# Kernel tuning notes

Hardware: AMD Instinct MI355X
Metric: run time of the kernel (lower is better)

## Reference

```python
import jax, jax.numpy as jnp
import numpy as np

N, K, B, D, T = 30000, 32, 8, 256, 10
NC = T + 1            # int_small_classes
LB_COL, UB_COL = 21, 22
INF = 1e18


def _ln(x, g, b, eps=1e-5):
    m = jnp.mean(x, axis=-1, keepdims=True)
    v = jnp.mean((x - m) ** 2, axis=-1, keepdims=True)
    return (x - m) * jax.lax.rsqrt(v + eps) * g + b


def _head(x, ng, nb, W1, b1, W2, b2, Wh, bh):
    # LayerNorm -> Linear -> GELU -> Linear -> GELU -> residual -> head (dropout off: eval)
    h = _ln(x, ng, nb)
    h = jax.nn.gelu(h @ W1.T + b1, approximate=False)
    h = jax.nn.gelu(h @ W2.T + b2, approximate=False)
    return (x + h) @ Wh.T + bh


def setup_inputs():
    key = jax.random.key(0)
    ks = jax.random.split(key, 32)
    s = 0.05
    inp = {}
    inp['evolved_tokens'] = jax.random.normal(ks[0], (B * K, D), jnp.float32)
    inp['var_batch'] = jnp.sort(jax.random.randint(ks[1], (N,), 0, B))
    aw = jax.random.uniform(ks[2], (N, K), jnp.float32)
    inp['attn_weights'] = aw / aw.sum(-1, keepdims=True)
    inp['var_types'] = jax.random.randint(ks[3], (N,), 0, 3)
    inp['z_var_0'] = jax.random.normal(ks[4], (N, D), jnp.float32)
    vf = 0.1 * jax.random.normal(ks[5], (N, 23), jnp.float32)
    lb = jnp.floor(jax.random.uniform(ks[6], (N,), minval=-5.0, maxval=0.0))
    ub = lb + jnp.floor(jax.random.uniform(ks[7], (N,), minval=0.0, maxval=30.0))
    ub = jnp.where(jax.random.uniform(ks[8], (N,)) < 0.1, 1e19, ub)
    inp['variable_features'] = vf.at[:, LB_COL].set(lb).at[:, UB_COL].set(ub)
    # deslice proj + fusion norm
    inp['Wp'] = s * jax.random.normal(ks[9], (D, D), jnp.float32)
    inp['bp'] = jnp.zeros((D,), jnp.float32)
    inp['fn_g'] = jnp.ones((D,), jnp.float32)
    inp['fn_b'] = jnp.zeros((D,), jnp.float32)
    # three decoder heads
    i = 10
    for name, out in (('bin', 1), ('ints', NC), ('intl', 1)):
        inp[name + '_ng'] = jnp.ones((D,), jnp.float32)
        inp[name + '_nb'] = jnp.zeros((D,), jnp.float32)
        inp[name + '_W1'] = s * jax.random.normal(ks[i], (D, D), jnp.float32)
        inp[name + '_b1'] = jnp.zeros((D,), jnp.float32)
        inp[name + '_W2'] = s * jax.random.normal(ks[i + 1], (D, D), jnp.float32)
        inp[name + '_b2'] = jnp.zeros((D,), jnp.float32)
        inp[name + '_Wh'] = s * jax.random.normal(ks[i + 2], (out, D), jnp.float32)
        inp[name + '_bh'] = (jnp.full((out,), -0.5, jnp.float32) if name == 'bin'
                             else jnp.zeros((out,), jnp.float32))
        i += 3
    return inp


def reference(evolved_tokens, var_batch, attn_weights, var_types, z_var_0,
              variable_features, Wp, bp, fn_g, fn_b,
              bin_ng, bin_nb, bin_W1, bin_b1, bin_W2, bin_b2, bin_Wh, bin_bh,
              ints_ng, ints_nb, ints_W1, ints_b1, ints_W2, ints_b2, ints_Wh, ints_bh,
              intl_ng, intl_nb, intl_W1, intl_b1, intl_W2, intl_b2, intl_Wh, intl_bh):
    # 1. deslice: attn_weights @ projected evolved tokens of the variable's graph
    proj = evolved_tokens @ Wp.T + bp          # [B*K, D]
    tok3 = proj.reshape(B, K, D)
    z_des = jnp.einsum('nk,nkd->nd', attn_weights, tok3[var_batch])  # [N, D]
    # 2. residual fusion + LayerNorm
    z_out = _ln(z_des + z_var_0, fn_g, fn_b)
    # 3. routing (extract_int_routing)
    lb = variable_features[:, LB_COL]
    ub = variable_features[:, UB_COL]
    is_int = var_types == 2
    finite = (jnp.abs(lb) < INF) & (jnp.abs(ub) < INF)
    mask_int_small = is_int & finite & ((ub - lb) <= T)
    mask_int_large = is_int & ~mask_int_small
    mask_bin = var_types == 1
    offsets = jnp.floor(lb)                                   # [N]
    ranges = jnp.clip(jnp.ceil(ub) - offsets + 1.0, 1.0, NC).astype(jnp.int32)  # [N]
    # 4. decode. Heads are evaluated densely on all N rows; the original's
    #    gather->MLP->scatter equals row-selection of these dense outputs.
    prob_bin = jax.nn.sigmoid(_head(z_out, bin_ng, bin_nb, bin_W1, bin_b1,
                                    bin_W2, bin_b2, bin_Wh, bin_bh))   # [N, 1]
    logits = _head(z_out, ints_ng, ints_nb, ints_W1, ints_b1,
                   ints_W2, ints_b2, ints_Wh, ints_bh)                 # [N, NC]
    valid = jnp.arange(NC)[None, :] < ranges[:, None]
    logits = jnp.where(valid, logits, -1e9)  # dynamic logit masking of invalid classes
    pred_large = _head(z_out, intl_ng, intl_nb, intl_W1, intl_b1,
                       intl_W2, intl_b2, intl_Wh, intl_bh)             # [N, 1]
    return (z_out, prob_bin, logits, pred_large,
            mask_bin, mask_int_small, mask_int_large, offsets, ranges)
```

## Files before the change

kernel.cpp:

```cpp
#include <hip/hip_runtime.h>
#include <math.h>

#define NV   30000
#define DD   256
#define KK   32
#define NCLS 11
#define NT   469
#define NT2  938

#define OZ  0
#define OPB 7680000
#define OLG 7710000
#define OPL 8040000
#define OMB 8070000
#define OMS 8100000
#define OML 8130000
#define OOF 8160000
#define ORG 8190000

typedef __bf16 bf16x8 __attribute__((ext_vector_type(8)));
typedef float  f32x4  __attribute__((ext_vector_type(4)));

__device__ __forceinline__ unsigned short f2b(float f) {
    unsigned u = __float_as_uint(f);
    u += 0x7fffu + ((u >> 16) & 1u);
    return (unsigned short)(u >> 16);
}

__device__ __forceinline__ float gelu_f(float x) {
    float x2 = x * x;
    float m = x * __builtin_fmaf(-0.0713548163f, x2, -1.5957691216f);
    float e = __expf(m);
    return x * __builtin_amdgcn_rcpf(1.0f + e);
}

__device__ __forceinline__ int swz(int row) {
    int r = row & 31;
    return (r + (r >> 3)) & 7;
}
__device__ __forceinline__ int lidx(int row, int col) {
    return row * 256 + ((((col) >> 3) ^ swz(row)) << 3) + (col & 7);
}
__device__ __forceinline__ int physchunk(int ck, int row) {
    return (ck & ~7) | ((ck & 7) ^ swz(row));
}

struct WP {
    const float *W1, *ng, *nb, *b1, *W2, *Wh;
    unsigned short *W1e, *W2b, *Whb;
    float *b1e, *swh;
    int nc;
};

__global__ void k_prep(const float* __restrict__ et, const float* __restrict__ Wp,
                       const float* __restrict__ bp, unsigned short* __restrict__ projT,
                       const float* __restrict__ vf, const int* __restrict__ vt,
                       float* __restrict__ out,
                       WP wa, WP wb, WP wc) {
    __shared__ float es[DD];
    __shared__ float red[4], red2[4];
    if (blockIdx.y == 0) {
        int r = blockIdx.x, c = threadIdx.x;
        es[c] = et[r * DD + c];
        __syncthreads();
        const float4* w4 = (const float4*)(Wp + c * DD);
        float acc = bp[c];
#pragma unroll 16
        for (int d = 0; d < DD / 4; ++d) {
            float4 w = w4[d];
            acc += es[4 * d] * w.x + es[4 * d + 1] * w.y + es[4 * d + 2] * w.z + es[4 * d + 3] * w.w;
        }
        projT[c * DD + r] = f2b(acc);
        return;
    }
    if (blockIdx.y == 4) {
        int n = blockIdx.x * 256 + threadIdx.x;
        if (n < NV) {
            float lb = vf[n * 23 + 21], ub = vf[n * 23 + 22];
            int t = vt[n];
            bool is_int = (t == 2);
            bool finite = (fabsf(lb) < 1e18f) && (fabsf(ub) < 1e18f);
            bool small_ = is_int && finite && (ub - lb <= 10.0f);
            float off = floorf(lb);
            float rngf = ceilf(ub) - off + 1.0f;
            rngf = fminf(fmaxf(rngf, 1.0f), (float)NCLS);
            out[OMB + n] = (t == 1) ? 1.0f : 0.0f;
            out[OMS + n] = small_ ? 1.0f : 0.0f;
            out[OML + n] = (is_int && !small_) ? 1.0f : 0.0f;
            out[OOF + n] = off;
            out[ORG + n] = (float)((int)rngf);
        }
        return;
    }
    WP wp = (blockIdx.y == 1) ? wa : ((blockIdx.y == 2) ? wb : wc);
    int j = blockIdx.x, d = threadIdx.x;
    float v1 = wp.W1[j * DD + d];
    wp.W1e[j * DD + d] = f2b(v1 * wp.ng[d]);
    wp.W2b[j * DD + d] = f2b(wp.W2[j * DD + d]);
    float p2 = 0.f;
    if (j < 16) {
        p2 = (j < wp.nc) ? wp.Wh[j * DD + d] : 0.f;
        wp.Whb[j * DD + d] = f2b(p2);
    }
    float p = v1 * wp.nb[d];
#pragma unroll
    for (int m = 1; m < 64; m <<= 1) { p += __shfl_xor(p, m); p2 += __shfl_xor(p2, m); }
    if ((d & 63) == 0) { red[d >> 6] = p; red2[d >> 6] = p2; }
    __syncthreads();
    if (d == 0) {
        wp.b1e[j] = wp.b1[j] + red[0] + red[1] + red[2] + red[3];
        if (j < 16) wp.swh[j] = red2[0] + red2[1] + red2[2] + red2[3];
    }
}

__global__ __launch_bounds__(512)
void k_zout(const unsigned short* __restrict__ projT, const int* __restrict__ vb,
            const float* __restrict__ aw, const float* __restrict__ z0,
            const float* __restrict__ g, const float* __restrict__ b,
            const unsigned short* __restrict__ Whb, const float* __restrict__ swh,
            float* __restrict__ out, unsigned short* __restrict__ zhat,
            float* __restrict__ zwhT) {
    __shared__ unsigned short Al[64 * 256];
    __shared__ float sqs[64 * 8], sqq[64 * 8];
    __shared__ float mvm[64], mvr[64], sig[64];
    __shared__ float gs[DD], bs[DD];
    __shared__ float swhs[48];
    int tid = threadIdx.x;
    int lane = tid & 63, wv = tid >> 6;
    int l15 = lane & 15, lq = lane >> 4;
    int n0 = blockIdx.x * 64;

    if (tid < 256) gs[tid] = g[tid];
    else           bs[tid - 256] = b[tid - 256];
    if (tid < 48) swhs[tid] = swh[tid];
    {
        uint4 z4 = make_uint4(0, 0, 0, 0);
        uint4* dst = (uint4*)Al;
#pragma unroll
        for (int j = 0; j < 4; ++j) dst[tid + j * 512] = z4;
    }
    __syncthreads();
    {
        int r = tid >> 3, sub = tid & 7;
        int n = n0 + r;
        if (n < NV) {
            int bb = vb[n];
            float4 a4 = *(const float4*)(aw + (size_t)n * KK + sub * 4);
            int j0 = bb * 32 + sub * 4;
            int phys = r * 256 + (physchunk(j0 >> 3, r) << 3) + (j0 & 7);
            ushort4 u;
            u.x = f2b(a4.x); u.y = f2b(a4.y); u.z = f2b(a4.z); u.w = f2b(a4.w);
            *(ushort4*)(Al + phys) = u;
        }
    }
    __syncthreads();

    int nb0 = wv * 32;
    f32x4 acc[4][2];
#pragma unroll
    for (int mt = 0; mt < 4; ++mt)
#pragma unroll
        for (int nt = 0; nt < 2; ++nt) acc[mt][nt] = f32x4{0.f, 0.f, 0.f, 0.f};

    {
        const unsigned short* Bb = projT + (size_t)(nb0 + l15) * DD + lq * 8;
        bf16x8 bfr[2][2], afr[4];
#pragma unroll
        for (int nt = 0; nt < 2; ++nt) bfr[0][nt] = *(const bf16x8*)(Bb + nt * 16 * DD);
#pragma unroll
        for (int ks = 0; ks < 8; ++ks) {
            int cur = ks & 1;
            if (ks < 7) {
#pragma unroll
                for (int nt = 0; nt < 2; ++nt)
                    bfr[cur ^ 1][nt] = *(const bf16x8*)(Bb + nt * 16 * DD + (ks + 1) * 32);
            }
            int ck = ks * 4 + lq;
#pragma unroll
            for (int mt = 0; mt < 4; ++mt) {
                int row = mt * 16 + l15;
                afr[mt] = *(const bf16x8*)(Al + row * 256 + (physchunk(ck, row) << 3));
            }
#pragma unroll
            for (int nt = 0; nt < 2; ++nt)
#pragma unroll
                for (int mt = 0; mt < 4; ++mt)
                    acc[mt][nt] = __builtin_amdgcn_mfma_f32_16x16x32_bf16(afr[mt], bfr[cur][nt], acc[mt][nt], 0, 0, 0);
        }
    }
#pragma unroll
    for (int mt = 0; mt < 4; ++mt)
#pragma unroll
        for (int nt = 0; nt < 2; ++nt) {
            int col = nb0 + nt * 16 + l15;
#pragma unroll
            for (int r = 0; r < 4; ++r) {
                int n = n0 + mt * 16 + lq * 4 + r;
                float zv = (n < NV) ? z0[(size_t)n * DD + col] : 0.f;
                acc[mt][nt][r] += zv;
            }
        }
#pragma unroll
    for (int mt = 0; mt < 4; ++mt)
#pragma unroll
        for (int r = 0; r < 4; ++r) {
            float s = acc[mt][0][r] + acc[mt][1][r];
            float q = acc[mt][0][r] * acc[mt][0][r] + acc[mt][1][r] * acc[mt][1][r];
#pragma unroll
            for (int m = 1; m < 16; m <<= 1) { s += __shfl_xor(s, m); q += __shfl_xor(q, m); }
            if (l15 == 0) { int row = mt * 16 + lq * 4 + r; sqs[row * 8 + wv] = s; sqq[row * 8 + wv] = q; }
        }
    __syncthreads();
    if (tid < 64) {
        float s = 0.f, q = 0.f;
#pragma unroll
        for (int w = 0; w < 8; ++w) { s += sqs[tid * 8 + w]; q += sqq[tid * 8 + w]; }
        float mean = s * (1.f / DD);
        float var  = q * (1.f / DD) - mean * mean;
        mvm[tid] = mean; mvr[tid] = rsqrtf(var + 1e-5f);
    }
    __syncthreads();
    float zb[4][2][4];
#pragma unroll
    for (int mt = 0; mt < 4; ++mt)
#pragma unroll
        for (int nt = 0; nt < 2; ++nt) {
            int col = nb0 + nt * 16 + l15;
#pragma unroll
            for (int r = 0; r < 4; ++r) {
                int row = mt * 16 + lq * 4 + r;
                float z = (acc[mt][nt][r] - mvm[row]) * mvr[row] * gs[col] + bs[col];
                zb[mt][nt][r] = z;
                int n = n0 + row;
                if (n < NV) out[OZ + (size_t)n * DD + col] = z;
            }
        }
#pragma unroll
    for (int mt = 0; mt < 4; ++mt)
#pragma unroll
        for (int r = 0; r < 4; ++r) {
            float s = zb[mt][0][r] + zb[mt][1][r];
            float q = zb[mt][0][r] * zb[mt][0][r] + zb[mt][1][r] * zb[mt][1][r];
#pragma unroll
            for (int m = 1; m < 16; m <<= 1) { s += __shfl_xor(s, m); q += __shfl_xor(q, m); }
            if (l15 == 0) { int row = mt * 16 + lq * 4 + r; sqs[row * 8 + wv] = s; sqq[row * 8 + wv] = q; }
        }
    __syncthreads();
    if (tid < 64) {
        float s = 0.f, q = 0.f;
#pragma unroll
        for (int w = 0; w < 8; ++w) { s += sqs[tid * 8 + w]; q += sqq[tid * 8 + w]; }
        float m2 = s * (1.f / DD);
        float v2 = q * (1.f / DD) - m2 * m2;
        float r2 = rsqrtf(v2 + 1e-5f);
        mvm[tid] = m2; mvr[tid] = r2; sig[tid] = (v2 + 1e-5f) * r2;
    }
    __syncthreads();
#pragma unroll
    for (int mt = 0; mt < 4; ++mt)
#pragma unroll
        for (int nt = 0; nt < 2; ++nt) {
            int col = nb0 + nt * 16 + l15;
#pragma unroll
            for (int r = 0; r < 4; ++r) {
                int row = mt * 16 + lq * 4 + r;
                Al[lidx(row, col)] = f2b((zb[mt][nt][r] - mvm[row]) * mvr[row]);
            }
        }
    __syncthreads();
    if (wv < 4) {
        f32x4 ac2[3];
#pragma unroll
        for (int mf = 0; mf < 3; ++mf) ac2[mf] = f32x4{0.f, 0.f, 0.f, 0.f};
        const unsigned short* Ab = Whb + (size_t)l15 * DD + lq * 8;
        int rowb = wv * 16 + l15;
#pragma unroll
        for (int ks = 0; ks < 8; ++ks) {
            int ck = ks * 4 + lq;
            bf16x8 bb2 = *(const bf16x8*)(Al + rowb * 256 + (physchunk(ck, rowb) << 3));
#pragma unroll
            for (int mf = 0; mf < 3; ++mf) {
                bf16x8 aa2 = *(const bf16x8*)(Ab + (size_t)mf * 16 * DD + ks * 32);
                ac2[mf] = __builtin_amdgcn_mfma_f32_16x16x32_bf16(aa2, bb2, ac2[mf], 0, 0, 0);
            }
        }
        int nl = wv * 16 + l15;
        float sg = sig[nl], mu = mvm[nl];
#pragma unroll
        for (int mf = 0; mf < 3; ++mf)
#pragma unroll
            for (int r = 0; r < 4; ++r) {
                int o = mf * 16 + lq * 4 + r;
                zwhT[(size_t)blockIdx.x * 3072 + o * 64 + nl] = sg * ac2[mf][r] + mu * swhs[o];
            }
    }
    {
        uint4* dstg = (uint4*)(zhat + (size_t)n0 * 256);
        const uint4* srcl = (const uint4*)Al;
#pragma unroll
        for (int j = 0; j < 4; ++j) dstg[tid + j * 512] = srcl[tid + j * 512];
    }
}

struct HeadP {
    const unsigned short *W1e, *W2b, *Whb;
    const float *b1e, *b2, *bh;
    int nc;
};

__global__ __launch_bounds__(512, 8)
void k_heads(const unsigned short* __restrict__ zhat, const float* __restrict__ zwhT,
             const float* __restrict__ ranges,
             HeadP h0, HeadP h1p, HeadP h2p,
             float* __restrict__ opb, float* __restrict__ olg, float* __restrict__ opl) {
    __shared__ unsigned short hl1[32 * 256];
    __shared__ unsigned short hl2[32 * 256];
    __shared__ float b1s[DD], b2s[DD];
    __shared__ float zws[16 * 32];
    __shared__ float rgs[32];
    __shared__ float bhs[16];

    int head = blockIdx.x / NT2;
    int tile = blockIdx.x % NT2;
    HeadP hp = (head == 0) ? h0 : ((head == 1) ? h1p : h2p);
    int nc = hp.nc;
    int n0 = tile * 32;
    int tid = threadIdx.x, lane = tid & 63, wv = tid >> 6;
    int l15 = lane & 15, lq = lane >> 4;
    int M0 = wv * 32;

    {
        const uint4* src = (const uint4*)(zhat + (size_t)n0 * 256);
        uint4* dst = (uint4*)hl1;
        dst[tid] = src[tid];
        dst[tid + 512] = src[tid + 512];
    }
    if (tid < 256) b1s[tid] = hp.b1e[tid];
    else           b2s[tid - 256] = hp.b2[tid - 256];
    {
        int t64 = tile >> 1, half = tile & 1;
        zws[tid & 511] = zwhT[(size_t)(t64 * 3 + head) * 1024 + (tid >> 5) * 64 + half * 32 + (tid & 31)];
    }
    if (tid < 32) { int n = n0 + tid; rgs[tid] = (n < NV) ? ranges[n] : 0.f; }
    else if (tid < 48) { int o = tid - 32; bhs[o] = (o < nc) ? hp.bh[o] : 0.f; }
    __syncthreads();

    f32x4 acc[2][2];
#pragma unroll
    for (int mt = 0; mt < 2; ++mt)
#pragma unroll
        for (int nt = 0; nt < 2; ++nt) acc[mt][nt] = f32x4{0.f, 0.f, 0.f, 0.f};

    {
        const unsigned short* Ab = hp.W1e + (size_t)(M0 + l15) * DD + lq * 8;
        bf16x8 afr[2][2], bfr[2];
#pragma unroll
        for (int mt = 0; mt < 2; ++mt) afr[0][mt] = *(const bf16x8*)(Ab + mt * 16 * DD);
#pragma unroll
        for (int ks = 0; ks < 8; ++ks) {
            int cur = ks & 1;
            if (ks < 7) {
#pragma unroll
                for (int mt = 0; mt < 2; ++mt)
                    afr[cur ^ 1][mt] = *(const bf16x8*)(Ab + mt * 16 * DD + (ks + 1) * 32);
            }
            int ck = ks * 4 + lq;
#pragma unroll
            for (int nt = 0; nt < 2; ++nt) {
                int row = nt * 16 + l15;
                bfr[nt] = *(const bf16x8*)(hl1 + row * 256 + (physchunk(ck, row) << 3));
            }
#pragma unroll
            for (int nt = 0; nt < 2; ++nt)
#pragma unroll
                for (int mt = 0; mt < 2; ++mt)
                    acc[mt][nt] = __builtin_amdgcn_mfma_f32_16x16x32_bf16(afr[cur][mt], bfr[nt], acc[mt][nt], 0, 0, 0);
        }
    }
#pragma unroll
    for (int mt = 0; mt < 2; ++mt) {
        int jb = M0 + mt * 16 + lq * 4;
        float4 bias = *(const float4*)(b1s + jb);
        int chunk = jb >> 3;
#pragma unroll
        for (int nt = 0; nt < 2; ++nt) {
            int n = nt * 16 + l15;
            ushort4 u;
            u.x = f2b(gelu_f(acc[mt][nt][0] + bias.x));
            u.y = f2b(gelu_f(acc[mt][nt][1] + bias.y));
            u.z = f2b(gelu_f(acc[mt][nt][2] + bias.z));
            u.w = f2b(gelu_f(acc[mt][nt][3] + bias.w));
            *(ushort4*)(hl2 + n * 256 + (physchunk(chunk, n) << 3) + (jb & 7)) = u;
        }
    }
    __syncthreads();

#pragma unroll
    for (int mt = 0; mt < 2; ++mt)
#pragma unroll
        for (int nt = 0; nt < 2; ++nt) acc[mt][nt] = f32x4{0.f, 0.f, 0.f, 0.f};
    {
        const unsigned short* Ab = hp.W2b + (size_t)(M0 + l15) * DD + lq * 8;
        bf16x8 afr[2][2], bfr[2];
#pragma unroll
        for (int mt = 0; mt < 2; ++mt) afr[0][mt] = *(const bf16x8*)(Ab + mt * 16 * DD);
#pragma unroll
        for (int ks = 0; ks < 8; ++ks) {
            int cur = ks & 1;
            if (ks < 7) {
#pragma unroll
                for (int mt = 0; mt < 2; ++mt)
                    afr[cur ^ 1][mt] = *(const bf16x8*)(Ab + mt * 16 * DD + (ks + 1) * 32);
            }
            int ck = ks * 4 + lq;
#pragma unroll
            for (int nt = 0; nt < 2; ++nt) {
                int row = nt * 16 + l15;
                bfr[nt] = *(const bf16x8*)(hl2 + row * 256 + (physchunk(ck, row) << 3));
            }
#pragma unroll
            for (int nt = 0; nt < 2; ++nt)
#pragma unroll
                for (int mt = 0; mt < 2; ++mt)
                    acc[mt][nt] = __builtin_amdgcn_mfma_f32_16x16x32_bf16(afr[cur][mt], bfr[nt], acc[mt][nt], 0, 0, 0);
        }
    }
#pragma unroll
    for (int mt = 0; mt < 2; ++mt) {
        int jb = M0 + mt * 16 + lq * 4;
        float4 bias = *(const float4*)(b2s + jb);
        int chunk = jb >> 3;
#pragma unroll
        for (int nt = 0; nt < 2; ++nt) {
            int n = nt * 16 + l15;
            ushort4 u;
            u.x = f2b(gelu_f(acc[mt][nt][0] + bias.x));
            u.y = f2b(gelu_f(acc[mt][nt][1] + bias.y));
            u.z = f2b(gelu_f(acc[mt][nt][2] + bias.z));
            u.w = f2b(gelu_f(acc[mt][nt][3] + bias.w));
            *(ushort4*)(hl1 + n * 256 + (physchunk(chunk, n) << 3) + (jb & 7)) = u;
        }
    }
    __syncthreads();

    f32x4 ap[2];
#pragma unroll
    for (int nt = 0; nt < 2; ++nt) ap[nt] = f32x4{0.f, 0.f, 0.f, 0.f};
    {
        bf16x8 afr = *(const bf16x8*)(hp.Whb + (size_t)l15 * DD + wv * 32 + lq * 8);
        int ck = wv * 4 + lq;
#pragma unroll
        for (int nt = 0; nt < 2; ++nt) {
            int row = nt * 16 + l15;
            bf16x8 bfr = *(const bf16x8*)(hl1 + row * 256 + (physchunk(ck, row) << 3));
            ap[nt] = __builtin_amdgcn_mfma_f32_16x16x32_bf16(afr, bfr, ap[nt], 0, 0, 0);
        }
    }
    {
        float* pb = (float*)hl2;
#pragma unroll
        for (int nt = 0; nt < 2; ++nt)
#pragma unroll
            for (int r = 0; r < 4; ++r)
                pb[wv * 512 + (lq * 4 + r) * 32 + nt * 16 + l15] = ap[nt][r];
    }
    __syncthreads();

    const float* pb = (const float*)hl2;
    for (int idx = tid; idx < 32 * nc; idx += 512) {
        int o = idx >> 5, n = idx & 31;
        float val = bhs[o] + zws[o * 32 + n];
#pragma unroll
        for (int w = 0; w < 8; ++w) val += pb[w * 512 + o * 32 + n];
        int ng = n0 + n;
        if (ng < NV) {
            if (head == 0)      opb[ng] = __builtin_amdgcn_rcpf(1.f + __expf(-val));
            else if (head == 2) opl[ng] = val;
            else {
                int rng = (int)rgs[n];
                olg[(size_t)ng * NCLS + o] = (o < rng) ? val : -1e9f;
            }
        }
    }
}

extern "C" void kernel_launch(void* const* d_in, const int* in_sizes, int n_in,
                              void* d_out, int out_size, void* d_ws, size_t ws_size,
                              hipStream_t stream) {
    const float* et = (const float*)d_in[0];
    const int*   vb = (const int*)d_in[1];
    const float* aw = (const float*)d_in[2];
    const int*   vt = (const int*)d_in[3];
    const float* z0 = (const float*)d_in[4];
    const float* vf = (const float*)d_in[5];
    const float* Wp = (const float*)d_in[6];
    const float* bp = (const float*)d_in[7];
    const float* fg = (const float*)d_in[8];
    const float* fb = (const float*)d_in[9];
    float* out = (float*)d_out;

    char* ws = (char*)d_ws;
    unsigned short* projT = (unsigned short*)ws;
    float* b1e           = (float*)(ws + 131072);
    unsigned short* W1e  = (unsigned short*)(ws + 134144);
    unsigned short* W2b  = (unsigned short*)(ws + 527360);
    unsigned short* Whb  = (unsigned short*)(ws + 920576);
    float* swh           = (float*)(ws + 945152);
    float* zwhT          = (float*)(ws + 945408);
    unsigned short* zhat = (unsigned short*)(ws + 6708480);

    WP wps[3];
    for (int h = 0; h < 3; ++h) {
        wps[h].W1 = (const float*)d_in[12 + 8 * h];
        wps[h].ng = (const float*)d_in[10 + 8 * h];
        wps[h].nb = (const float*)d_in[11 + 8 * h];
        wps[h].b1 = (const float*)d_in[13 + 8 * h];
        wps[h].W2 = (const float*)d_in[14 + 8 * h];
        wps[h].Wh = (const float*)d_in[16 + 8 * h];
        wps[h].W1e = W1e + h * 65536;
        wps[h].W2b = W2b + h * 65536;
        wps[h].Whb = Whb + h * 4096;
        wps[h].b1e = b1e + h * 256;
        wps[h].swh = swh + h * 16;
        wps[h].nc  = (h == 1) ? NCLS : 1;
    }
    k_prep<<<dim3(256, 5), 256, 0, stream>>>(et, Wp, bp, projT, vf, vt, out,
                                             wps[0], wps[1], wps[2]);

    k_zout<<<NT, 512, 0, stream>>>(projT, vb, aw, z0, fg, fb, Whb, swh,
                                   out, zhat, zwhT);

    HeadP hps[3];
    for (int h = 0; h < 3; ++h) {
        hps[h].W1e = W1e + h * 65536;
        hps[h].W2b = W2b + h * 65536;
        hps[h].Whb = Whb + h * 4096;
        hps[h].b1e = b1e + h * 256;
        hps[h].b2  = (const float*)d_in[15 + 8 * h];
        hps[h].bh  = (const float*)d_in[17 + 8 * h];
        hps[h].nc  = (h == 1) ? NCLS : 1;
    }
    k_heads<<<3 * NT2, 512, 0, stream>>>(zhat, zwhT, out + ORG,
                                         hps[0], hps[1], hps[2],
                                         out + OPB, out + OLG, out + OPL);
}
```

Baseline: 278.6 us.

## Restructure head kernel to 256 threads with one shared buffer; skip zero batch blocks

The head kernel moves from 512 to 256 threads per block, so each wave computes a 64-row output slice instead of 32. It reuses a single shared activation buffer in place, with extra barriers and a tile-dependent swizzle offset, and reads biases and ranges straight from global memory instead of staging them. The z_out kernel limits its K loop to the batch chunks present in the tile (bmin..bmax), which relies on var_batch being sorted and skips MFMAs on zero attention blocks. The projection dot product in the prep kernel is split into four independent accumulators. The risk is lost software prefetch of weight fragments and extra synchronisation in exchange for lower LDS use.

```diff
diff --git a/kernel.cpp b/kernel.cpp
--- a/kernel.cpp
+++ b/kernel.cpp
@@ -34,10 +34,7 @@
     return x * __builtin_amdgcn_rcpf(1.0f + e);
 }
 
-__device__ __forceinline__ int swz(int row) {
-    int r = row & 31;
-    return (r + (r >> 3)) & 7;
-}
+__device__ __forceinline__ int swz(int row) { return (row + (row >> 3)) & 7; }
 __device__ __forceinline__ int lidx(int row, int col) {
     return row * 256 + ((((col) >> 3) ^ swz(row)) << 3) + (col & 7);
 }
@@ -64,12 +61,16 @@
         es[c] = et[r * DD + c];
         __syncthreads();
         const float4* w4 = (const float4*)(Wp + c * DD);
-        float acc = bp[c];
+        float a0 = 0.f, a1 = 0.f, a2 = 0.f, a3 = 0.f;
 #pragma unroll 16
         for (int d = 0; d < DD / 4; ++d) {
             float4 w = w4[d];
-            acc += es[4 * d] * w.x + es[4 * d + 1] * w.y + es[4 * d + 2] * w.z + es[4 * d + 3] * w.w;
-        }
+            a0 += es[4 * d] * w.x;
+            a1 += es[4 * d + 1] * w.y;
+            a2 += es[4 * d + 2] * w.z;
+            a3 += es[4 * d + 3] * w.w;
+        }
+        float acc = bp[c] + ((a0 + a1) + (a2 + a3));
         projT[c * DD + r] = f2b(acc);
         return;
     }
@@ -130,6 +131,9 @@
     int l15 = lane & 15, lq = lane >> 4;
     int n0 = blockIdx.x * 64;
 
+    int bmin = vb[n0];
+    int bmax = vb[(n0 + 63 < NV) ? (n0 + 63) : (NV - 1)];
+
     if (tid < 256) gs[tid] = g[tid];
     else           bs[tid - 256] = b[tid - 256];
     if (tid < 48) swhs[tid] = swh[tid];
@@ -164,28 +168,20 @@
 
     {
         const unsigned short* Bb = projT + (size_t)(nb0 + l15) * DD + lq * 8;
-        bf16x8 bfr[2][2], afr[4];
-#pragma unroll
-        for (int nt = 0; nt < 2; ++nt) bfr[0][nt] = *(const bf16x8*)(Bb + nt * 16 * DD);
-#pragma unroll
-        for (int ks = 0; ks < 8; ++ks) {
-            int cur = ks & 1;
-            if (ks < 7) {
-#pragma unroll
-                for (int nt = 0; nt < 2; ++nt)
-                    bfr[cur ^ 1][nt] = *(const bf16x8*)(Bb + nt * 16 * DD + (ks + 1) * 32);
-            }
+        for (int ks = bmin; ks <= bmax; ++ks) {
+            bf16x8 bfr[2];
+#pragma unroll
+            for (int nt = 0; nt < 2; ++nt)
+                bfr[nt] = *(const bf16x8*)(Bb + nt * 16 * DD + ks * 32);
             int ck = ks * 4 + lq;
 #pragma unroll
             for (int mt = 0; mt < 4; ++mt) {
                 int row = mt * 16 + l15;
-                afr[mt] = *(const bf16x8*)(Al + row * 256 + (physchunk(ck, row) << 3));
-            }
-#pragma unroll
-            for (int nt = 0; nt < 2; ++nt)
-#pragma unroll
-                for (int mt = 0; mt < 4; ++mt)
-                    acc[mt][nt] = __builtin_amdgcn_mfma_f32_16x16x32_bf16(afr[mt], bfr[cur][nt], acc[mt][nt], 0, 0, 0);
+                bf16x8 afr = *(const bf16x8*)(Al + row * 256 + (physchunk(ck, row) << 3));
+#pragma unroll
+                for (int nt = 0; nt < 2; ++nt)
+                    acc[mt][nt] = __builtin_amdgcn_mfma_f32_16x16x32_bf16(afr, bfr[nt], acc[mt][nt], 0, 0, 0);
+            }
         }
     }
 #pragma unroll
@@ -308,137 +304,124 @@
     int nc;
 };
 
-__global__ __launch_bounds__(512, 8)
+__global__ __launch_bounds__(256, 5)
 void k_heads(const unsigned short* __restrict__ zhat, const float* __restrict__ zwhT,
              const float* __restrict__ ranges,
              HeadP h0, HeadP h1p, HeadP h2p,
              float* __restrict__ opb, float* __restrict__ olg, float* __restrict__ opl) {
-    __shared__ unsigned short hl1[32 * 256];
-    __shared__ unsigned short hl2[32 * 256];
+    __shared__ unsigned short hl[32 * 256];
     __shared__ float b1s[DD], b2s[DD];
-    __shared__ float zws[16 * 32];
-    __shared__ float rgs[32];
-    __shared__ float bhs[16];
 
     int head = blockIdx.x / NT2;
     int tile = blockIdx.x % NT2;
     HeadP hp = (head == 0) ? h0 : ((head == 1) ? h1p : h2p);
     int nc = hp.nc;
     int n0 = tile * 32;
+    int sadd = (tile & 1) << 2;
     int tid = threadIdx.x, lane = tid & 63, wv = tid >> 6;
     int l15 = lane & 15, lq = lane >> 4;
-    int M0 = wv * 32;
+    int M0 = wv * 64;
 
     {
         const uint4* src = (const uint4*)(zhat + (size_t)n0 * 256);
-        uint4* dst = (uint4*)hl1;
-        dst[tid] = src[tid];
-        dst[tid + 512] = src[tid + 512];
-    }
-    if (tid < 256) b1s[tid] = hp.b1e[tid];
-    else           b2s[tid - 256] = hp.b2[tid - 256];
-    {
-        int t64 = tile >> 1, half = tile & 1;
-        zws[tid & 511] = zwhT[(size_t)(t64 * 3 + head) * 1024 + (tid >> 5) * 64 + half * 32 + (tid & 31)];
-    }
-    if (tid < 32) { int n = n0 + tid; rgs[tid] = (n < NV) ? ranges[n] : 0.f; }
-    else if (tid < 48) { int o = tid - 32; bhs[o] = (o < nc) ? hp.bh[o] : 0.f; }
-    __syncthreads();
-
-    f32x4 acc[2][2];
-#pragma unroll
-    for (int mt = 0; mt < 2; ++mt)
+        uint4* dst = (uint4*)hl;
+#pragma unroll
+        for (int j = 0; j < 4; ++j) dst[tid + j * 256] = src[tid + j * 256];
+    }
+    b1s[tid] = hp.b1e[tid];
+    b2s[tid] = hp.b2[tid];
+    __syncthreads();
+
+    f32x4 acc[4][2];
+#pragma unroll
+    for (int mt = 0; mt < 4; ++mt)
 #pragma unroll
         for (int nt = 0; nt < 2; ++nt) acc[mt][nt] = f32x4{0.f, 0.f, 0.f, 0.f};
 
     {
         const unsigned short* Ab = hp.W1e + (size_t)(M0 + l15) * DD + lq * 8;
-        bf16x8 afr[2][2], bfr[2];
-#pragma unroll
-        for (int mt = 0; mt < 2; ++mt) afr[0][mt] = *(const bf16x8*)(Ab + mt * 16 * DD);
 #pragma unroll
         for (int ks = 0; ks < 8; ++ks) {
-            int cur = ks & 1;
-            if (ks < 7) {
-#pragma unroll
-                for (int mt = 0; mt < 2; ++mt)
-                    afr[cur ^ 1][mt] = *(const bf16x8*)(Ab + mt * 16 * DD + (ks + 1) * 32);
-            }
             int ck = ks * 4 + lq;
+            bf16x8 bfr[2];
 #pragma unroll
             for (int nt = 0; nt < 2; ++nt) {
                 int row = nt * 16 + l15;
-                bfr[nt] = *(const bf16x8*)(hl1 + row * 256 + (physchunk(ck, row) << 3));
-            }
-#pragma unroll
-            for (int nt = 0; nt < 2; ++nt)
-#pragma unroll
-                for (int mt = 0; mt < 2; ++mt)
-                    acc[mt][nt] = __builtin_amdgcn_mfma_f32_16x16x32_bf16(afr[cur][mt], bfr[nt], acc[mt][nt], 0, 0, 0);
-        }
-    }
-#pragma unroll
-    for (int mt = 0; mt < 2; ++mt) {
+                int chunk = (ck & ~7) | ((ck & 7) ^ ((swz(row) + sadd) & 7));
+                bfr[nt] = *(const bf16x8*)(hl + row * 256 + (chunk << 3));
+            }
+#pragma unroll
+            for (int mt = 0; mt < 4; ++mt) {
+                bf16x8 afr = *(const bf16x8*)(Ab + mt * 16 * DD + ks * 32);
+#pragma unroll
+                for (int nt = 0; nt < 2; ++nt)
+                    acc[mt][nt] = __builtin_amdgcn_mfma_f32_16x16x32_bf16(afr, bfr[nt], acc[mt][nt], 0, 0, 0);
+            }
+        }
+    }
+    __syncthreads();
+
+#pragma unroll
+    for (int mt = 0; mt < 4; ++mt) {
         int jb = M0 + mt * 16 + lq * 4;
         float4 bias = *(const float4*)(b1s + jb);
-        int chunk = jb >> 3;
+        int ckj = jb >> 3;
 #pragma unroll
         for (int nt = 0; nt < 2; ++nt) {
             int n = nt * 16 + l15;
+            int chunk = (ckj & ~7) | ((ckj & 7) ^ ((swz(n) + sadd) & 7));
             ushort4 u;
             u.x = f2b(gelu_f(acc[mt][nt][0] + bias.x));
             u.y = f2b(gelu_f(acc[mt][nt][1] + bias.y));
             u.z = f2b(gelu_f(acc[mt][nt][2] + bias.z));
             u.w = f2b(gelu_f(acc[mt][nt][3] + bias.w));
-            *(ushort4*)(hl2 + n * 256 + (physchunk(chunk, n) << 3) + (jb & 7)) = u;
-        }
-    }
-    __syncthreads();
-
-#pragma unroll
-    for (int mt = 0; mt < 2; ++mt)
+            *(ushort4*)(hl + n * 256 + (chunk << 3) + (jb & 7)) = u;
+        }
+    }
+    __syncthreads();
+
+#pragma unroll
+    for (int mt = 0; mt < 4; ++mt)
 #pragma unroll
         for (int nt = 0; nt < 2; ++nt) acc[mt][nt] = f32x4{0.f, 0.f, 0.f, 0.f};
     {
         const unsigned short* Ab = hp.W2b + (size_t)(M0 + l15) * DD + lq * 8;
-        bf16x8 afr[2][2], bfr[2];
-#pragma unroll
-        for (int mt = 0; mt < 2; ++mt) afr[0][mt] = *(const bf16x8*)(Ab + mt * 16 * DD);
 #pragma unroll
         for (int ks = 0; ks < 8; ++ks) {
-            int cur = ks & 1;
-            if (ks < 7) {
-#pragma unroll
-                for (int mt = 0; mt < 2; ++mt)
-                    afr[cur ^ 1][mt] = *(const bf16x8*)(Ab + mt * 16 * DD + (ks + 1) * 32);
-            }
             int ck = ks * 4 + lq;
+            bf16x8 bfr[2];
 #pragma unroll
             for (int nt = 0; nt < 2; ++nt) {
                 int row = nt * 16 + l15;
-                bfr[nt] = *(const bf16x8*)(hl2 + row * 256 + (physchunk(ck, row) << 3));
-            }
-#pragma unroll
-            for (int nt = 0; nt < 2; ++nt)
-#pragma unroll
-                for (int mt = 0; mt < 2; ++mt)
-                    acc[mt][nt] = __builtin_amdgcn_mfma_f32_16x16x32_bf16(afr[cur][mt], bfr[nt], acc[mt][nt], 0, 0, 0);
-        }
-    }
-#pragma unroll
-    for (int mt = 0; mt < 2; ++mt) {
+                int chunk = (ck & ~7) | ((ck & 7) ^ ((swz(row) + sadd) & 7));
+                bfr[nt] = *(const bf16x8*)(hl + row * 256 + (chunk << 3));
+            }
+#pragma unroll
+            for (int mt = 0; mt < 4; ++mt) {
+                bf16x8 afr = *(const bf16x8*)(Ab + mt * 16 * DD + ks * 32);
+#pragma unroll
+                for (int nt = 0; nt < 2; ++nt)
+                    acc[mt][nt] = __builtin_amdgcn_mfma_f32_16x16x32_bf16(afr, bfr[nt], acc[mt][nt], 0, 0, 0);
+            }
+        }
+    }
+    __syncthreads();
+
+#pragma unroll
+    for (int mt = 0; mt < 4; ++mt) {
         int jb = M0 + mt * 16 + lq * 4;
         float4 bias = *(const float4*)(b2s + jb);
-        int chunk = jb >> 3;
+        int ckj = jb >> 3;
 #pragma unroll
         for (int nt = 0; nt < 2; ++nt) {
             int n = nt * 16 + l15;
+            int chunk = (ckj & ~7) | ((ckj & 7) ^ ((swz(n) + sadd) & 7));
             ushort4 u;
             u.x = f2b(gelu_f(acc[mt][nt][0] + bias.x));
             u.y = f2b(gelu_f(acc[mt][nt][1] + bias.y));
             u.z = f2b(gelu_f(acc[mt][nt][2] + bias.z));
             u.w = f2b(gelu_f(acc[mt][nt][3] + bias.w));
-            *(ushort4*)(hl1 + n * 256 + (physchunk(chunk, n) << 3) + (jb & 7)) = u;
+            *(ushort4*)(hl + n * 256 + (chunk << 3) + (jb & 7)) = u;
         }
     }
     __syncthreads();
@@ -447,17 +430,24 @@
 #pragma unroll
     for (int nt = 0; nt < 2; ++nt) ap[nt] = f32x4{0.f, 0.f, 0.f, 0.f};
     {
-        bf16x8 afr = *(const bf16x8*)(hp.Whb + (size_t)l15 * DD + wv * 32 + lq * 8);
-        int ck = wv * 4 + lq;
-#pragma unroll
-        for (int nt = 0; nt < 2; ++nt) {
-            int row = nt * 16 + l15;
-            bf16x8 bfr = *(const bf16x8*)(hl1 + row * 256 + (physchunk(ck, row) << 3));
-            ap[nt] = __builtin_amdgcn_mfma_f32_16x16x32_bf16(afr, bfr, ap[nt], 0, 0, 0);
-        }
-    }
-    {
-        float* pb = (float*)hl2;
+        const unsigned short* Wb = hp.Whb + (size_t)l15 * DD + wv * 64 + lq * 8;
+#pragma unroll
+        for (int kh = 0; kh < 2; ++kh) {
+            bf16x8 afr = *(const bf16x8*)(Wb + kh * 32);
+            int ck = wv * 8 + kh * 4 + lq;
+#pragma unroll
+            for (int nt = 0; nt < 2; ++nt) {
+                int row = nt * 16 + l15;
+                int chunk = (ck & ~7) | ((ck & 7) ^ ((swz(row) + sadd) & 7));
+                bf16x8 bfr = *(const bf16x8*)(hl + row * 256 + (chunk << 3));
+                ap[nt] = __builtin_amdgcn_mfma_f32_16x16x32_bf16(afr, bfr, ap[nt], 0, 0, 0);
+            }
+        }
+    }
+    __syncthreads();
+
+    {
+        float* pb = (float*)hl;
 #pragma unroll
         for (int nt = 0; nt < 2; ++nt)
 #pragma unroll
@@ -466,18 +456,20 @@
     }
     __syncthreads();
 
-    const float* pb = (const float*)hl2;
-    for (int idx = tid; idx < 32 * nc; idx += 512) {
+    const float* pb = (const float*)hl;
+    int t64 = tile >> 1, half = tile & 1;
+    const float* zwt = zwhT + (size_t)(t64 * 3 + head) * 1024 + half * 32;
+    for (int idx = tid; idx < 32 * nc; idx += 256) {
         int o = idx >> 5, n = idx & 31;
-        float val = bhs[o] + zws[o * 32 + n];
-#pragma unroll
-        for (int w = 0; w < 8; ++w) val += pb[w * 512 + o * 32 + n];
+        float val = hp.bh[o] + zwt[o * 64 + n];
+#pragma unroll
+        for (int w = 0; w < 4; ++w) val += pb[w * 512 + o * 32 + n];
         int ng = n0 + n;
         if (ng < NV) {
             if (head == 0)      opb[ng] = __builtin_amdgcn_rcpf(1.f + __expf(-val));
             else if (head == 2) opl[ng] = val;
             else {
-                int rng = (int)rgs[n];
+                int rng = (int)ranges[ng];
                 olg[(size_t)ng * NCLS + o] = (o < rng) ? val : -1e9f;
             }
         }
@@ -540,7 +532,7 @@
         hps[h].bh  = (const float*)d_in[17 + 8 * h];
         hps[h].nc  = (h == 1) ? NCLS : 1;
     }
-    k_heads<<<3 * NT2, 512, 0, stream>>>(zhat, zwhT, out + ORG,
+    k_heads<<<3 * NT2, 256, 0, stream>>>(zhat, zwhT, out + ORG,
                                          hps[0], hps[1], hps[2],
                                          out + OPB, out + OLG, out + OPL);
 }
```

Result: no change. 273.4 us (-1.9%).
